# Kernel tuning notes

Hardware: AMD Instinct MI355X
Metric: run time of the kernel (lower is better)

Reference implementation:

```python
import jax, jax.numpy as jnp
import numpy as np
from jax import lax

EPS = 1e-5

def silu(x):
    return x * jax.nn.sigmoid(x)

def rms_norm(x, w):
    return x * lax.rsqrt(jnp.mean(x * x, axis=-1, keepdims=True) + EPS) * w

def causal_dwconv(x, w, b):
    # x: (B, L, d), w: (d, K) depthwise causal conv, pad left K-1
    K = w.shape[1]
    L = x.shape[1]
    xp = jnp.pad(x, ((0, 0), (K - 1, 0), (0, 0)))
    y = sum(w[:, k] * xp[:, k:k + L, :] for k in range(K))
    return y + b

def selective_scan(xs_in, dt, Bm, Cm, A):
    # xs_in, dt: (B, L, d); Bm, Cm: (B, L, n); A: (d, n)
    Bsz, L, d = xs_in.shape
    n = A.shape[1]

    def step(h, inp):
        dt_t, B_t, C_t, x_t = inp  # (B,d),(B,n),(B,n),(B,d)
        dA = jnp.exp(dt_t[:, :, None] * A)            # (B,d,n)
        h = h * dA + (dt_t * x_t)[:, :, None] * B_t[:, None, :]
        y = jnp.einsum('bdn,bn->bd', h, C_t)
        return h, y

    xs = (jnp.swapaxes(dt, 0, 1), jnp.swapaxes(Bm, 0, 1),
          jnp.swapaxes(Cm, 0, 1), jnp.swapaxes(xs_in, 0, 1))
    h0 = jnp.zeros((Bsz, d, n), xs_in.dtype)
    _, ys = lax.scan(step, h0, xs)
    return jnp.swapaxes(ys, 0, 1)  # (B, L, d)

def mamba1(x, nw, ipw, cw, cb, xpw, dtw, dtb, Alog, Dp, opw):
    # Block: out = mixer(rmsnorm(x)); caller adds residual x.
    xn = rms_norm(x, nw)
    xz = xn @ ipw.T                      # (B,L,2d)
    d = ipw.shape[0] // 2
    xc, z = xz[..., :d], xz[..., d:]
    xc = silu(causal_dwconv(xc, cw, cb))
    dbl = xc @ xpw.T                     # (B,L,r+2n)
    r = dtw.shape[1]
    n = Alog.shape[1]
    dt = jax.nn.softplus(dbl[..., :r] @ dtw.T + dtb)  # (B,L,d)
    Bm = dbl[..., r:r + n]
    Cm = dbl[..., r + n:r + 2 * n]
    A = -jnp.exp(Alog)
    y = selective_scan(xc, dt, Bm, Cm, A)
    y = y + Dp * xc
    y = y * silu(z)
    return y @ opw.T

def mamba_bidir(x, P, i_f, i_b):
    # P: tuple of stacked param arrays; indices select direction-specific params
    (nw, ipw, cw, cb, xpw, dtw, dtb, Alog, Dp, opw) = P

    def m(xx, i):
        return mamba1(xx, nw[i], ipw[i], cw[i], cb[i], xpw[i],
                      dtw[i], dtb[i], Alog[i], Dp[i], opw[i])

    yf = x + m(x, i_f)
    xb = x[:, ::-1, :]
    yb = (xb + m(xb, i_b))[:, ::-1, :]
    return jnp.concatenate([yf, yb], axis=-1)  # (B, L, 2c)

def tf_mamba(x, norm_w, in_proj_w, conv_w, conv_b, x_proj_w, dt_proj_w,
             dt_proj_b, A_log, D, out_proj_w, tlin_w, tlin_b, flin_w, flin_b):
    b, c, t, f = x.shape
    P = (norm_w, in_proj_w, conv_w, conv_b, x_proj_w, dt_proj_w, dt_proj_b,
         A_log, D, out_proj_w)
    xt = jnp.transpose(x, (0, 3, 2, 1)).reshape(b * f, t, c)
    xt = mamba_bidir(xt, P, 0, 1) @ tlin_w + tlin_b + xt
    xf = xt.reshape(b, f, t, c).transpose(0, 2, 1, 3).reshape(b * t, f, c)
    xf = mamba_bidir(xf, P, 2, 3) @ flin_w + flin_b + xf
    return xf.reshape(b, t, f, c).transpose(0, 3, 1, 2)

def setup_inputs() -> dict:
    key = jax.random.key(0)
    b, c, t, f = 1, 64, 128, 128
    expand, n, K = 4, 16, 4
    d = expand * c            # 256
    r = (c + 15) // 16        # dt_rank = 4
    ks = jax.random.split(key, 12)
    f32 = jnp.float32

    # dt bias init as in Mamba: dt ~ exp(U(log 1e-3, log 0.1)); bias = softplus^-1(dt)
    dt = jnp.exp(jax.random.uniform(ks[0], (4, d)) *
                 (np.log(0.1) - np.log(0.001)) + np.log(0.001))
    dt_proj_b = dt + jnp.log(-jnp.expm1(-dt))

    inp = {
        'x': jax.random.normal(ks[1], (b, c, t, f), f32),
        'norm_w': jnp.ones((4, c), f32),
        'in_proj_w': jax.random.normal(ks[2], (4, 2 * d, c), f32) * 0.02,
        'conv_w': jax.random.normal(ks[3], (4, d, K), f32) * (1.0 / np.sqrt(K)),
        'conv_b': jnp.zeros((4, d), f32),
        'x_proj_w': jax.random.normal(ks[4], (4, r + 2 * n, d), f32) * 0.02,
        'dt_proj_w': jax.random.normal(ks[5], (4, d, r), f32) * (r ** -0.5),
        'dt_proj_b': dt_proj_b.astype(f32),
        'A_log': jnp.log(jnp.broadcast_to(
            jnp.arange(1, n + 1, dtype=f32), (4, d, n))).copy(),
        'D': jnp.ones((4, d), f32),
        'out_proj_w': jax.random.normal(ks[6], (4, c, d), f32) * 0.02,
        'tlin_w': jax.random.normal(ks[7], (2 * c, c), f32) * 0.02,
        'tlin_b': jnp.zeros((c,), f32),
        'flin_w': jax.random.normal(ks[8], (2 * c, c), f32) * 0.02,
        'flin_b': jnp.zeros((c,), f32),
    }
    return inp

def reference(x, norm_w, in_proj_w, conv_w, conv_b, x_proj_w, dt_proj_w,
              dt_proj_b, A_log, D, out_proj_w, tlin_w, tlin_b, flin_w, flin_b):
    return tf_mamba(x, norm_w, in_proj_w, conv_w, conv_b, x_proj_w, dt_proj_w,
                    dt_proj_b, A_log, D, out_proj_w, tlin_w, tlin_b, flin_w,
                    flin_b)
```

## Files before the change

### kernel.cpp

```cpp
#include <hip/hip_runtime.h>
#include <math.h>

#define LSEQ 128
#define NROW 128
#define POS (LSEQ*NROW)
#define CDIM 64
#define DDIM 256
#define NSTATE 16
#define RDIM 4
#define KCONV 4

static __forceinline__ __device__ float dot4(float4 a, float4 b) {
    return a.x*b.x + a.y*b.y + a.z*b.z + a.w*b.w;
}

__global__ __launch_bounds__(256) void k_prep1(const float* __restrict__ x,
                                               float* __restrict__ seq_in) {
    __shared__ float tile[64][65];
    int t   = blockIdx.x & 127;
    int fi0 = (blockIdx.x >> 7) << 6;
    int lane = threadIdx.x & 63;
    int r    = threadIdx.x >> 6;
    #pragma unroll
    for (int i = 0; i < 16; i++) {
        int cc = 4*i + r;
        tile[cc][lane] = x[cc*16384 + t*128 + fi0 + lane];
    }
    __syncthreads();
    #pragma unroll
    for (int i = 0; i < 16; i++) {
        int fl = 4*i + r;
        seq_in[(fi0 + fl)*8192 + t*64 + lane] = tile[lane][fl];
    }
}

__global__ __launch_bounds__(256) void k_final(const float* __restrict__ s,
                                               float* __restrict__ outp) {
    __shared__ float tile[64][65];
    int t   = blockIdx.x & 127;
    int fi0 = (blockIdx.x >> 7) << 6;
    int lane = threadIdx.x & 63;
    int r    = threadIdx.x >> 6;
    #pragma unroll
    for (int i = 0; i < 16; i++) {
        int fl = 4*i + r;
        tile[fl][lane] = s[(((t << 7) + fi0 + fl) << 6) + lane];
    }
    __syncthreads();
    #pragma unroll
    for (int i = 0; i < 16; i++) {
        int cc = 4*i + r;
        outp[cc*16384 + (t << 7) + fi0 + lane] = tile[lane][cc];
    }
}

__global__ __launch_bounds__(128) void k_inproj(const float* __restrict__ seq_in,
                                                const float* __restrict__ nw_s,
                                                const float* __restrict__ ipw_s,
                                                float* __restrict__ xc_pre,
                                                float* __restrict__ zbuf) {
    __shared__ float xn[16][64];
    int dir = blockIdx.x >> 10;
    int g0  = (blockIdx.x & 1023) << 4;
    size_t dirOff = (size_t)dir * POS * DDIM;
    const float* nw  = nw_s  + dir*CDIM;
    const float* ipw = ipw_s + (size_t)dir * 2*DDIM*CDIM;

    int wv   = threadIdx.x >> 6;
    int lane = threadIdx.x & 63;
    float nwv = nw[lane];
    #pragma unroll
    for (int pi = wv; pi < 16; pi += 2) {
        int p = g0 + pi;
        int row = p >> 7, tau = p & 127;
        int s = dir ? (127 - tau) : tau;
        int q = (row << 7) + s;
        float v = seq_in[(q << 6) + lane];
        float ss = v*v;
        #pragma unroll
        for (int off = 32; off; off >>= 1) ss += __shfl_xor(ss, off, 64);
        float rs = rsqrtf(ss*(1.0f/64.0f) + 1e-5f);
        xn[pi][lane] = v*rs*nwv;
    }
    __syncthreads();

    int j = threadIdx.x;
    const float4* w0p = (const float4*)(ipw + (j << 6));
    const float4* w1p = (const float4*)(ipw + ((j + 128) << 6));
    const float4* w2p = (const float4*)(ipw + ((j + 256) << 6));
    const float4* w3p = (const float4*)(ipw + ((j + 384) << 6));
    float acc0[16], acc1[16], acc2[16], acc3[16];
    #pragma unroll
    for (int i = 0; i < 16; i++) { acc0[i] = 0.f; acc1[i] = 0.f; acc2[i] = 0.f; acc3[i] = 0.f; }
    #pragma unroll 4
    for (int k4 = 0; k4 < 16; k4++) {
        float4 wa = w0p[k4], wb = w1p[k4], wc = w2p[k4], wd = w3p[k4];
        #pragma unroll
        for (int i = 0; i < 16; i++) {
            float4 xv = *((const float4*)&xn[i][k4 << 2]);
            acc0[i] += dot4(wa, xv);
            acc1[i] += dot4(wb, xv);
            acc2[i] += dot4(wc, xv);
            acc3[i] += dot4(wd, xv);
        }
    }
    #pragma unroll
    for (int i = 0; i < 16; i++) {
        size_t base = dirOff + (size_t)(g0 + i)*DDIM;
        xc_pre[base + j]       = acc0[i];
        xc_pre[base + j + 128] = acc1[i];
        zbuf  [base + j]       = acc2[i];
        zbuf  [base + j + 128] = acc3[i];
    }
}

__global__ __launch_bounds__(256) void k_convxproj(const float* __restrict__ xc_pre,
                                                   const float* __restrict__ cw_s,
                                                   const float* __restrict__ cb_s,
                                                   const float* __restrict__ xpw_s,
                                                   float* __restrict__ xcb,
                                                   float* __restrict__ dblg) {
    __shared__ float lx[16][260];
    int dir = blockIdx.x >> 10;
    int g0  = (blockIdx.x & 1023) << 4;
    int tau0 = g0 & 127;
    size_t dirOff = (size_t)dir * POS * DDIM;
    const float* cw  = cw_s  + dir*DDIM*KCONV;
    const float* cb  = cb_s  + dir*DDIM;
    const float* xpw = xpw_s + (size_t)dir*36*DDIM;
    int t = threadIdx.x;

    float r[19];
    #pragma unroll
    for (int j = 0; j < 19; j++) {
        r[j] = (tau0 == 0 && j < 3) ? 0.f
             : xc_pre[dirOff + (size_t)(g0 - 3 + j)*DDIM + t];
    }
    float c0 = cw[t*4], c1 = cw[t*4+1], c2 = cw[t*4+2], c3 = cw[t*4+3];
    float cbv = cb[t];
    #pragma unroll
    for (int i = 0; i < 16; i++) {
        float a = cbv + c0*r[i] + c1*r[i+1] + c2*r[i+2] + c3*r[i+3];
        float sv = a / (1.f + __expf(-a));
        lx[i][t] = sv;
        xcb[dirOff + (size_t)(g0 + i)*DDIM + t] = sv;
    }
    __syncthreads();

    #pragma unroll
    for (int rep = 0; rep < 3; rep++) {
        int oid = rep*256 + t;
        if (oid < 576) {
            int pos = oid & 15;
            int j   = oid >> 4;
            const float4* xr = (const float4*)&lx[pos][0];
            const float4* wr = (const float4*)(xpw + (j << 8));
            float a0 = 0.f, a1 = 0.f, a2 = 0.f, a3 = 0.f;
            #pragma unroll 4
            for (int k4 = 0; k4 < 64; k4 += 4) {
                float4 xv0 = xr[k4],   wv0 = wr[k4];
                float4 xv1 = xr[k4+1], wv1 = wr[k4+1];
                float4 xv2 = xr[k4+2], wv2 = wr[k4+2];
                float4 xv3 = xr[k4+3], wv3 = wr[k4+3];
                a0 += dot4(wv0, xv0);
                a1 += dot4(wv1, xv1);
                a2 += dot4(wv2, xv2);
                a3 += dot4(wv3, xv3);
            }
            dblg[(size_t)dir*POS*36 + (size_t)(g0 + pos)*36 + j] =
                (a0 + a1) + (a2 + a3);
        }
    }
}

__global__ __launch_bounds__(512) void k_scan(const float* __restrict__ xc,
                                              const float* __restrict__ dblg,
                                              const float* __restrict__ dtw_s,
                                              const float* __restrict__ dtb_s,
                                              const float* __restrict__ Alog_s,
                                              const float* __restrict__ Dp_s,
                                              const float* __restrict__ zbuf,
                                              float* __restrict__ y) {
    __shared__ float sdbl[128*36];
    int dir  = blockIdx.x >> 7;
    int row  = blockIdx.x & 127;
    int ch   = threadIdx.x >> 1;
    int half = threadIdx.x & 1;
    int s0   = half << 3;
    size_t dirOff = (size_t)dir * POS * DDIM;
    const float* Alog = Alog_s + dir*DDIM*NSTATE;
    const float* Dp   = Dp_s   + dir*DDIM;
    const float* dtw  = dtw_s  + dir*DDIM*RDIM;
    const float* dtb  = dtb_s  + dir*DDIM;

    {
        const float4* src = (const float4*)(dblg + (size_t)dir*POS*36
                                            + (size_t)row*128*36);
        float4* dst = (float4*)sdbl;
        for (int i = threadIdx.x; i < 128*36/4; i += 512) dst[i] = src[i];
    }
    float a[8], h[8];
    #pragma unroll
    for (int j = 0; j < 8; j++) {
        a[j] = -__expf(Alog[ch*16 + s0 + j]);
        h[j] = 0.f;
    }
    float dv = Dp[ch];
    float tw0 = dtw[ch*4], tw1 = dtw[ch*4+1], tw2 = dtw[ch*4+2], tw3 = dtw[ch*4+3];
    float tb  = dtb[ch];
    __syncthreads();

    size_t off = dirOff + ((size_t)row*128)*DDIM + ch;
    const size_t ybase = off;
    float x0 = xc[off],        z0 = zbuf[off];
    float x1 = xc[off + DDIM], z1 = zbuf[off + DDIM];
    for (int tau = 0; tau < 128; tau++) {
        float x2 = 0.f, z2 = 0.f;
        if (tau + 2 < 128) {
            size_t offn = off + 2*DDIM;
            x2 = xc[offn]; z2 = zbuf[offn];
        }
        const float* db = &sdbl[tau*36];
        float adt = tb + db[0]*tw0 + db[1]*tw1 + db[2]*tw2 + db[3]*tw3;
        float dtv = (adt > 0.f) ? (adt + log1pf(__expf(-adt)))
                                : log1pf(__expf(adt));
        float dtx = dtv*x0;
        const float* B = db + 4 + s0;
        const float* C = db + 20 + s0;
        float ac0 = 0.f, ac1 = 0.f, ac2 = 0.f, ac3 = 0.f;
        #pragma unroll
        for (int j = 0; j < 8; j += 4) {
            float dA0 = __expf(dtv*a[j]);
            float dA1 = __expf(dtv*a[j+1]);
            float dA2 = __expf(dtv*a[j+2]);
            float dA3 = __expf(dtv*a[j+3]);
            h[j]   = h[j]*dA0   + dtx*B[j];
            h[j+1] = h[j+1]*dA1 + dtx*B[j+1];
            h[j+2] = h[j+2]*dA2 + dtx*B[j+2];
            h[j+3] = h[j+3]*dA3 + dtx*B[j+3];
            ac0 += h[j]*C[j];
            ac1 += h[j+1]*C[j+1];
            ac2 += h[j+2]*C[j+2];
            ac3 += h[j+3]*C[j+3];
        }
        float acc = (ac0 + ac1) + (ac2 + ac3);
        acc += __shfl_xor(acc, 1, 64);
        if (!half) {
            float yv = acc + dv*x0;
            yv *= z0 / (1.f + __expf(-z0));
            int s = dir ? (127 - tau) : tau;
            y[ybase + (size_t)s*DDIM] = yv;
        }
        x0 = x1; z0 = z1; x1 = x2; z1 = z2; off += DDIM;
    }
}

__global__ __launch_bounds__(256) void k_outlin(const float* __restrict__ y,
                                                const float* __restrict__ opw_s,
                                                const float* __restrict__ seq_in,
                                                const float* __restrict__ lw,
                                                const float* __restrict__ lb,
                                                float* __restrict__ seq_out,
                                                int twrite) {
    __shared__ float cat[32][128];
    int tid = threadIdx.x;
    int g0  = blockIdx.x << 5;

    {
        int cc  = tid & 63;
        int q   = tid >> 6;
        int dir = q & 1;
        int pg  = q >> 1;
        int p0  = g0 + (pg << 4);
        const float* yb = y + (size_t)dir*POS*DDIM + (size_t)p0*DDIM;
        const float4* wp = (const float4*)(opw_s + (size_t)dir*CDIM*DDIM
                                           + (size_t)cc*DDIM);
        float acc[16];
        #pragma unroll
        for (int i = 0; i < 16; i++) acc[i] = 0.f;
        for (int k4 = 0; k4 < 64; k4++) {
            float4 w = wp[k4];
            #pragma unroll
            for (int i = 0; i < 16; i++) {
                float4 xv = *((const float4*)(yb + (size_t)i*DDIM + (k4 << 2)));
                acc[i] += dot4(w, xv);
            }
        }
        #pragma unroll
        for (int i = 0; i < 16; i++) {
            float siv = seq_in[(size_t)(p0 + i)*CDIM + cc];
            cat[(pg << 4) + i][(dir << 6) + cc] = siv + acc[i];
        }
    }
    __syncthreads();

    {
        int cc  = tid & 63;
        int grp = tid >> 6;
        int ib  = grp << 3;
        float bv = lb[cc];
        float acc2[8];
        #pragma unroll
        for (int ii = 0; ii < 8; ii++) acc2[ii] = bv;
        for (int k4 = 0; k4 < 32; k4++) {
            int k = k4 << 2;
            float w0 = lw[(k + 0)*64 + cc];
            float w1 = lw[(k + 1)*64 + cc];
            float w2 = lw[(k + 2)*64 + cc];
            float w3 = lw[(k + 3)*64 + cc];
            #pragma unroll
            for (int ii = 0; ii < 8; ii++) {
                float4 cv = *((const float4*)&cat[ib + ii][k]);
                acc2[ii] += cv.x*w0 + cv.y*w1 + cv.z*w2 + cv.w*w3;
            }
        }
        #pragma unroll
        for (int ii = 0; ii < 8; ii++) {
            int p = g0 + ib + ii;
            float val = acc2[ii] + seq_in[(size_t)p*CDIM + cc];
            if (twrite) {
                int dstp = ((p & 127) << 7) + (p >> 7);
                seq_out[((size_t)dstp << 6) + cc] = val;
            } else {
                seq_out[((size_t)p << 6) + cc] = val;
            }
        }
    }
}

extern "C" void kernel_launch(void* const* d_in, const int* in_sizes, int n_in,
                              void* d_out, int out_size, void* d_ws, size_t ws_size,
                              hipStream_t stream) {
    (void)in_sizes; (void)n_in; (void)out_size; (void)ws_size;
    const float* x      = (const float*)d_in[0];
    const float* norm_w = (const float*)d_in[1];
    const float* ipw    = (const float*)d_in[2];
    const float* cw     = (const float*)d_in[3];
    const float* cb     = (const float*)d_in[4];
    const float* xpw    = (const float*)d_in[5];
    const float* dtw    = (const float*)d_in[6];
    const float* dtbp   = (const float*)d_in[7];
    const float* Alog   = (const float*)d_in[8];
    const float* Dp     = (const float*)d_in[9];
    const float* opw    = (const float*)d_in[10];
    const float* tlw    = (const float*)d_in[11];
    const float* tlb    = (const float*)d_in[12];
    const float* flw    = (const float*)d_in[13];
    const float* flb    = (const float*)d_in[14];
    float* outp = (float*)d_out;

    float* ws       = (float*)d_ws;
    float* seq_in   = ws;
    float* xc_pre   = seq_in  + (size_t)POS*64;
    float* zbuf     = xc_pre  + (size_t)2*POS*256;
    float* xcb      = zbuf    + (size_t)2*POS*256;
    float* dblbuf   = xcb     + (size_t)2*POS*256;
    float* seq_out  = dblbuf  + (size_t)2*POS*36;

    auto stage = [&](int st, const float* lw, const float* lb, int twrite,
                     float* sout) {
        int pi = 2*st;
        k_inproj   <<<2*POS/16, 128, 0, stream>>>(seq_in,
                        norm_w + pi*CDIM, ipw + (size_t)pi*2*DDIM*CDIM,
                        xc_pre, zbuf);
        k_convxproj<<<2*POS/16, 256, 0, stream>>>(xc_pre,
                        cw + pi*DDIM*KCONV, cb + pi*DDIM,
                        xpw + (size_t)pi*36*DDIM,
                        xcb, dblbuf);
        k_scan     <<<2*NROW, 512, 0, stream>>>(xcb, dblbuf,
                        dtw + pi*DDIM*RDIM, dtbp + pi*DDIM,
                        Alog + (size_t)pi*DDIM*NSTATE, Dp + pi*DDIM,
                        zbuf, xc_pre);
        k_outlin   <<<POS/32, 256, 0, stream>>>(xc_pre,
                        opw + (size_t)pi*CDIM*DDIM, seq_in, lw, lb,
                        sout, twrite);
    };

    k_prep1<<<256, 256, 0, stream>>>(x, seq_in);
    stage(0, tlw, tlb, 1, seq_out);

    {
        float* tmp = seq_in; seq_in = seq_out; seq_out = tmp;
    }
    stage(1, flw, flb, 0, seq_out);

    k_final<<<256, 256, 0, stream>>>(seq_out, outp);
}
```

Before: 677.4 us.

## Move dt projection and softplus into conv kernel; split scan across four lanes per channel

After: 634.1 us. -6.4%, faster.

```diff
diff --git a/kernel.cpp b/kernel.cpp
--- a/kernel.cpp
+++ b/kernel.cpp
@@ -12,6 +12,9 @@
 
 static __forceinline__ __device__ float dot4(float4 a, float4 b) {
     return a.x*b.x + a.y*b.y + a.z*b.z + a.w*b.w;
+}
+static __forceinline__ __device__ float fast_silu(float v) {
+    return v * __builtin_amdgcn_rcpf(1.f + __expf(-v));
 }
 
 __global__ __launch_bounds__(256) void k_prep1(const float* __restrict__ x,
@@ -118,9 +121,13 @@
                                                    const float* __restrict__ cw_s,
                                                    const float* __restrict__ cb_s,
                                                    const float* __restrict__ xpw_s,
+                                                   const float* __restrict__ dtw_s,
+                                                   const float* __restrict__ dtb_s,
                                                    float* __restrict__ xcb,
+                                                   float* __restrict__ dtout,
                                                    float* __restrict__ dblg) {
     __shared__ float lx[16][260];
+    __shared__ float rq[16][4];
     int dir = blockIdx.x >> 10;
     int g0  = (blockIdx.x & 1023) << 4;
     int tau0 = g0 & 127;
@@ -128,6 +135,8 @@
     const float* cw  = cw_s  + dir*DDIM*KCONV;
     const float* cb  = cb_s  + dir*DDIM;
     const float* xpw = xpw_s + (size_t)dir*36*DDIM;
+    const float* dtw = dtw_s + dir*DDIM*RDIM;
+    const float* dtb = dtb_s + dir*DDIM;
     int t = threadIdx.x;
 
     float r[19];
@@ -141,7 +150,7 @@
     #pragma unroll
     for (int i = 0; i < 16; i++) {
         float a = cbv + c0*r[i] + c1*r[i+1] + c2*r[i+2] + c3*r[i+3];
-        float sv = a / (1.f + __expf(-a));
+        float sv = fast_silu(a);
         lx[i][t] = sv;
         xcb[dirOff + (size_t)(g0 + i)*DDIM + t] = sv;
     }
@@ -167,91 +176,84 @@
                 a2 += dot4(wv2, xv2);
                 a3 += dot4(wv3, xv3);
             }
-            dblg[(size_t)dir*POS*36 + (size_t)(g0 + pos)*36 + j] =
-                (a0 + a1) + (a2 + a3);
-        }
-    }
-}
-
-__global__ __launch_bounds__(512) void k_scan(const float* __restrict__ xc,
-                                              const float* __restrict__ dblg,
-                                              const float* __restrict__ dtw_s,
-                                              const float* __restrict__ dtb_s,
-                                              const float* __restrict__ Alog_s,
-                                              const float* __restrict__ Dp_s,
-                                              const float* __restrict__ zbuf,
-                                              float* __restrict__ y) {
-    __shared__ float sdbl[128*36];
-    int dir  = blockIdx.x >> 7;
-    int row  = blockIdx.x & 127;
-    int ch   = threadIdx.x >> 1;
-    int half = threadIdx.x & 1;
-    int s0   = half << 3;
+            float v = (a0 + a1) + (a2 + a3);
+            if (j < 4) rq[pos][j] = v;
+            else dblg[(size_t)dir*POS*32 + (size_t)(g0 + pos)*32 + (j - 4)] = v;
+        }
+    }
+    __syncthreads();
+
+    float dbv = dtb[t];
+    float4 tw = *((const float4*)(dtw + t*4));
+    #pragma unroll
+    for (int i = 0; i < 16; i++) {
+        float a = dbv + rq[i][0]*tw.x + rq[i][1]*tw.y + rq[i][2]*tw.z + rq[i][3]*tw.w;
+        float sp = (a > 0.f) ? (a + log1pf(__expf(-a))) : log1pf(__expf(a));
+        dtout[dirOff + (size_t)(g0 + i)*DDIM + t] = sp;
+    }
+}
+
+__global__ __launch_bounds__(1024) void k_scan(const float* __restrict__ xc,
+                                               const float* __restrict__ dt,
+                                               const float* __restrict__ dblg,
+                                               const float* __restrict__ Alog_s,
+                                               const float* __restrict__ Dp_s,
+                                               const float* __restrict__ zbuf,
+                                               float* __restrict__ y) {
+    __shared__ float sbc[128*32];
+    int dir = blockIdx.x >> 7;
+    int row = blockIdx.x & 127;
+    int ch  = threadIdx.x >> 2;
+    int q   = threadIdx.x & 3;
+    int s0  = q << 2;
     size_t dirOff = (size_t)dir * POS * DDIM;
     const float* Alog = Alog_s + dir*DDIM*NSTATE;
     const float* Dp   = Dp_s   + dir*DDIM;
-    const float* dtw  = dtw_s  + dir*DDIM*RDIM;
-    const float* dtb  = dtb_s  + dir*DDIM;
 
     {
-        const float4* src = (const float4*)(dblg + (size_t)dir*POS*36
-                                            + (size_t)row*128*36);
-        float4* dst = (float4*)sdbl;
-        for (int i = threadIdx.x; i < 128*36/4; i += 512) dst[i] = src[i];
-    }
-    float a[8], h[8];
-    #pragma unroll
-    for (int j = 0; j < 8; j++) {
-        a[j] = -__expf(Alog[ch*16 + s0 + j]);
-        h[j] = 0.f;
-    }
+        const float4* src = (const float4*)(dblg + (size_t)dir*POS*32
+                                            + (size_t)row*128*32);
+        float4* dst = (float4*)sbc;
+        for (int i = threadIdx.x; i < 128*32/4; i += 1024) dst[i] = src[i];
+    }
+    float4 av = *((const float4*)(Alog + ch*16 + s0));
+    float a0 = -__expf(av.x), a1 = -__expf(av.y);
+    float a2 = -__expf(av.z), a3 = -__expf(av.w);
+    float h0 = 0.f, h1 = 0.f, h2 = 0.f, h3 = 0.f;
     float dv = Dp[ch];
-    float tw0 = dtw[ch*4], tw1 = dtw[ch*4+1], tw2 = dtw[ch*4+2], tw3 = dtw[ch*4+3];
-    float tb  = dtb[ch];
     __syncthreads();
 
     size_t off = dirOff + ((size_t)row*128)*DDIM + ch;
     const size_t ybase = off;
-    float x0 = xc[off],        z0 = zbuf[off];
-    float x1 = xc[off + DDIM], z1 = zbuf[off + DDIM];
+    float x0 = xc[off],        z0 = zbuf[off],        d0 = dt[off];
+    float x1 = xc[off + DDIM], z1 = zbuf[off + DDIM], d1 = dt[off + DDIM];
     for (int tau = 0; tau < 128; tau++) {
-        float x2 = 0.f, z2 = 0.f;
+        float x2 = 0.f, z2 = 0.f, d2 = 0.f;
         if (tau + 2 < 128) {
             size_t offn = off + 2*DDIM;
-            x2 = xc[offn]; z2 = zbuf[offn];
-        }
-        const float* db = &sdbl[tau*36];
-        float adt = tb + db[0]*tw0 + db[1]*tw1 + db[2]*tw2 + db[3]*tw3;
-        float dtv = (adt > 0.f) ? (adt + log1pf(__expf(-adt)))
-                                : log1pf(__expf(adt));
+            x2 = xc[offn]; z2 = zbuf[offn]; d2 = dt[offn];
+        }
+        float dtv = d0;
         float dtx = dtv*x0;
-        const float* B = db + 4 + s0;
-        const float* C = db + 20 + s0;
-        float ac0 = 0.f, ac1 = 0.f, ac2 = 0.f, ac3 = 0.f;
-        #pragma unroll
-        for (int j = 0; j < 8; j += 4) {
-            float dA0 = __expf(dtv*a[j]);
-            float dA1 = __expf(dtv*a[j+1]);
-            float dA2 = __expf(dtv*a[j+2]);
-            float dA3 = __expf(dtv*a[j+3]);
-            h[j]   = h[j]*dA0   + dtx*B[j];
-            h[j+1] = h[j+1]*dA1 + dtx*B[j+1];
-            h[j+2] = h[j+2]*dA2 + dtx*B[j+2];
-            h[j+3] = h[j+3]*dA3 + dtx*B[j+3];
-            ac0 += h[j]*C[j];
-            ac1 += h[j+1]*C[j+1];
-            ac2 += h[j+2]*C[j+2];
-            ac3 += h[j+3]*C[j+3];
-        }
-        float acc = (ac0 + ac1) + (ac2 + ac3);
+        float4 B = *((const float4*)&sbc[tau*32 + s0]);
+        float4 C = *((const float4*)&sbc[tau*32 + 16 + s0]);
+        float dA0 = __expf(dtv*a0);
+        float dA1 = __expf(dtv*a1);
+        float dA2 = __expf(dtv*a2);
+        float dA3 = __expf(dtv*a3);
+        h0 = h0*dA0 + dtx*B.x;
+        h1 = h1*dA1 + dtx*B.y;
+        h2 = h2*dA2 + dtx*B.z;
+        h3 = h3*dA3 + dtx*B.w;
+        float acc = (h0*C.x + h1*C.y) + (h2*C.z + h3*C.w);
         acc += __shfl_xor(acc, 1, 64);
-        if (!half) {
-            float yv = acc + dv*x0;
-            yv *= z0 / (1.f + __expf(-z0));
+        acc += __shfl_xor(acc, 2, 64);
+        if (q == 0) {
+            float yv = (acc + dv*x0) * fast_silu(z0);
             int s = dir ? (127 - tau) : tau;
             y[ybase + (size_t)s*DDIM] = yv;
         }
-        x0 = x1; z0 = z1; x1 = x2; z1 = z2; off += DDIM;
+        x0 = x1; z0 = z1; d0 = d1; x1 = x2; z1 = z2; d1 = d2; off += DDIM;
     }
 }
 
@@ -354,8 +356,9 @@
     float* xc_pre   = seq_in  + (size_t)POS*64;
     float* zbuf     = xc_pre  + (size_t)2*POS*256;
     float* xcb      = zbuf    + (size_t)2*POS*256;
-    float* dblbuf   = xcb     + (size_t)2*POS*256;
-    float* seq_out  = dblbuf  + (size_t)2*POS*36;
+    float* dtbuf    = xcb     + (size_t)2*POS*256;
+    float* dblbuf   = dtbuf   + (size_t)2*POS*256;
+    float* seq_out  = dblbuf  + (size_t)2*POS*32;
 
     auto stage = [&](int st, const float* lw, const float* lb, int twrite,
                      float* sout) {
@@ -366,9 +369,9 @@
         k_convxproj<<<2*POS/16, 256, 0, stream>>>(xc_pre,
                         cw + pi*DDIM*KCONV, cb + pi*DDIM,
                         xpw + (size_t)pi*36*DDIM,
-                        xcb, dblbuf);
-        k_scan     <<<2*NROW, 512, 0, stream>>>(xcb, dblbuf,
                         dtw + pi*DDIM*RDIM, dtbp + pi*DDIM,
+                        xcb, dtbuf, dblbuf);
+        k_scan     <<<2*NROW, 1024, 0, stream>>>(xcb, dtbuf, dblbuf,
                         Alog + (size_t)pi*DDIM*NSTATE, Dp + pi*DDIM,
                         zbuf, xc_pre);
         k_outlin   <<<POS/32, 256, 0, stream>>>(xc_pre,
```
